# Performance work log

Hardware: AMD Instinct MI355X
Metric: run time of the kernel (lower is better)

The kernel has to match this reference:

```python
import jax, jax.numpy as jnp
import numpy as np

H = 1024   # hidden_size
F = 2048   # feature_length (encoder steps)
V = 50257  # output vocab size


def setup_inputs() -> dict:
    key = jax.random.key(0)
    ks = jax.random.split(key, 16)
    s = 0.02
    return {
        "input_tok": jax.random.randint(ks[0], (1,), 0, V, dtype=jnp.int32),
        "hidden": jax.random.normal(ks[1], (1, 1, H), dtype=jnp.float32),
        "encoder_output": jax.random.normal(ks[2], (1, F, H), dtype=jnp.float32),
        "emb": jax.random.normal(ks[3], (V, H), dtype=jnp.float32) * s,
        "attn_W": jax.random.normal(ks[4], (F, 2 * H), dtype=jnp.float32) * s,
        "attn_b": jnp.zeros((F,), dtype=jnp.float32),
        "comb_W": jax.random.normal(ks[5], (H, 2 * H), dtype=jnp.float32) * s,
        "comb_b": jnp.zeros((H,), dtype=jnp.float32),
        "W_ih": jax.random.normal(ks[6], (3 * H, H), dtype=jnp.float32) * s,
        "W_hh": jax.random.normal(ks[7], (3 * H, H), dtype=jnp.float32) * s,
        "b_ih": jnp.zeros((3 * H,), dtype=jnp.float32),
        "b_hh": jnp.zeros((3 * H,), dtype=jnp.float32),
        "out_W": jax.random.normal(ks[8], (V, H), dtype=jnp.float32) * s,
        "out_b": jnp.zeros((V,), dtype=jnp.float32),
    }


def reference(input_tok, hidden, encoder_output, emb, attn_W, attn_b,
              comb_W, comb_b, W_ih, W_hh, b_ih, b_hh, out_W, out_b):
    # embedding lookup -> [1, H] (dropout is identity in eval mode)
    embedded = emb[input_tok]                                   # [1, H]
    h = hidden[0]                                               # [1, H]
    # attention weights over encoder steps
    cat1 = jnp.concatenate([embedded, h], axis=1)               # [1, 2H]
    attn_weights = jax.nn.softmax(cat1 @ attn_W.T + attn_b, axis=1)  # [1, F]
    # weighted sum of encoder outputs
    attn_applied = attn_weights @ encoder_output[0]             # [1, H]
    # combine + relu
    cat2 = jnp.concatenate([embedded, attn_applied], axis=1)    # [1, 2H]
    x = jax.nn.relu(cat2 @ comb_W.T + comb_b)                   # [1, H]
    # single GRU step (torch gate order: r, z, n)
    gx = x @ W_ih.T + b_ih                                      # [1, 3H]
    gh = h @ W_hh.T + b_hh                                      # [1, 3H]
    r = jax.nn.sigmoid(gx[:, :H] + gh[:, :H])
    z = jax.nn.sigmoid(gx[:, H:2 * H] + gh[:, H:2 * H])
    n = jnp.tanh(gx[:, 2 * H:] + r * gh[:, 2 * H:])
    h_new = (1.0 - z) * n + z * h                               # [1, H]
    # output projection + log-softmax
    out = jax.nn.log_softmax(h_new @ out_W.T + out_b, axis=1)   # [1, V]
    return out, h_new[None], attn_weights
```

## Files before the change

### kernel.cpp

```cpp
#include <hip/hip_runtime.h>
#include <math.h>

#define H 1024
#define F 2048
#define V 50257

#define WS_ATTNL   0
#define WS_APPLIED 2048
#define WS_X       3072
#define WS_HNEW    4096
#define WS_LOGITS  5120
#define WS_STATS   55380

__device__ __forceinline__ float wave_sum(float v) {
    #pragma unroll
    for (int off = 32; off > 0; off >>= 1) v += __shfl_xor(v, off, 64);
    return v;
}

__device__ __forceinline__ float dot4(float4 a, float4 b) {
    return a.x * b.x + a.y * b.y + a.z * b.z + a.w * b.w;
}

__global__ void k_attn(const int* __restrict__ tok_p, const float* __restrict__ hidden,
                       const float* __restrict__ emb, const float* __restrict__ attn_W,
                       const float* __restrict__ attn_b, float* __restrict__ logits) {
    const int wv = threadIdx.x >> 6, lane = threadIdx.x & 63;
    const int f = blockIdx.x * 4 + wv;
    const int tok = tok_p[0];
    const float4* e4 = (const float4*)(emb + (size_t)tok * H);
    const float4* h4 = (const float4*)hidden;
    const float4* row = (const float4*)(attn_W + (size_t)f * (2 * H));
    float acc = 0.f;
    #pragma unroll
    for (int k = lane; k < H / 4; k += 64) acc += dot4(e4[k], row[k]);
    #pragma unroll
    for (int k = lane; k < H / 4; k += 64) acc += dot4(h4[k], row[H / 4 + k]);
    acc = wave_sum(acc);
    if (lane == 0) logits[f] = acc + attn_b[f];
}

__global__ void k_softmax(const float* __restrict__ logits, float* __restrict__ weights,
                          float* __restrict__ applied) {
    __shared__ float red[16];
    __shared__ float bc;
    const int t = threadIdx.x, lane = t & 63, wv = t >> 6;
    applied[t] = 0.f;
    float x0 = logits[t], x1 = logits[t + 1024];
    float m = fmaxf(x0, x1);
    #pragma unroll
    for (int off = 32; off > 0; off >>= 1) m = fmaxf(m, __shfl_xor(m, off, 64));
    if (lane == 0) red[wv] = m;
    __syncthreads();
    if (t == 0) { float M = red[0]; for (int w = 1; w < 16; ++w) M = fmaxf(M, red[w]); bc = M; }
    __syncthreads();
    const float M = bc;
    float e0 = expf(x0 - M), e1 = expf(x1 - M);
    float s = wave_sum(e0 + e1);
    if (lane == 0) red[wv] = s;
    __syncthreads();
    if (t == 0) { float S = red[0]; for (int w = 1; w < 16; ++w) S += red[w]; bc = 1.f / S; }
    __syncthreads();
    const float inv = bc;
    weights[t] = e0 * inv;
    weights[t + 1024] = e1 * inv;
}

__global__ void k_attnapply(const float* __restrict__ weights, const float* __restrict__ enc,
                            float* __restrict__ applied) {
    const int h = blockIdx.x * 256 + threadIdx.x;
    const int f0 = blockIdx.y * 32;
    float acc = 0.f;
    #pragma unroll 8
    for (int f = f0; f < f0 + 32; ++f) acc += weights[f] * enc[(size_t)f * H + h];
    atomicAdd(&applied[h], acc);
}

__global__ void k_comb(const int* __restrict__ tok_p, const float* __restrict__ emb,
                       const float* __restrict__ applied, const float* __restrict__ comb_W,
                       const float* __restrict__ comb_b, float* __restrict__ x) {
    const int wv = threadIdx.x >> 6, lane = threadIdx.x & 63;
    const int i = blockIdx.x * 4 + wv;
    const int tok = tok_p[0];
    const float4* e4 = (const float4*)(emb + (size_t)tok * H);
    const float4* a4 = (const float4*)applied;
    const float4* row = (const float4*)(comb_W + (size_t)i * (2 * H));
    float acc = 0.f;
    #pragma unroll
    for (int k = lane; k < H / 4; k += 64) acc += dot4(e4[k], row[k]);
    #pragma unroll
    for (int k = lane; k < H / 4; k += 64) acc += dot4(a4[k], row[H / 4 + k]);
    acc = wave_sum(acc);
    if (lane == 0) x[i] = fmaxf(acc + comb_b[i], 0.f);
}

__global__ void k_gru(const float* __restrict__ x, const float* __restrict__ hidden,
                      const float* __restrict__ W_ih, const float* __restrict__ W_hh,
                      const float* __restrict__ b_ih, const float* __restrict__ b_hh,
                      float* __restrict__ hnew_out, float* __restrict__ hnew_ws) {
    const int wv = threadIdx.x >> 6, lane = threadIdx.x & 63;
    const int i = blockIdx.x * 4 + wv;
    const float4* x4 = (const float4*)x;
    const float4* h4 = (const float4*)hidden;
    const float4* wri = (const float4*)(W_ih + (size_t)i * H);
    const float4* wzi = (const float4*)(W_ih + (size_t)(H + i) * H);
    const float4* wni = (const float4*)(W_ih + (size_t)(2 * H + i) * H);
    const float4* wrh = (const float4*)(W_hh + (size_t)i * H);
    const float4* wzh = (const float4*)(W_hh + (size_t)(H + i) * H);
    const float4* wnh = (const float4*)(W_hh + (size_t)(2 * H + i) * H);
    float ar = 0.f, az = 0.f, an = 0.f, br = 0.f, bz = 0.f, bn = 0.f;
    #pragma unroll
    for (int k = lane; k < H / 4; k += 64) {
        float4 xv = x4[k], hv = h4[k];
        ar += dot4(xv, wri[k]);
        az += dot4(xv, wzi[k]);
        an += dot4(xv, wni[k]);
        br += dot4(hv, wrh[k]);
        bz += dot4(hv, wzh[k]);
        bn += dot4(hv, wnh[k]);
    }
    ar = wave_sum(ar); az = wave_sum(az); an = wave_sum(an);
    br = wave_sum(br); bz = wave_sum(bz); bn = wave_sum(bn);
    if (lane == 0) {
        float r = 1.f / (1.f + expf(-((ar + b_ih[i]) + (br + b_hh[i]))));
        float z = 1.f / (1.f + expf(-((az + b_ih[H + i]) + (bz + b_hh[H + i]))));
        float n = tanhf((an + b_ih[2 * H + i]) + r * (bn + b_hh[2 * H + i]));
        float hn = (1.f - z) * n + z * hidden[i];
        hnew_out[i] = hn;
        hnew_ws[i] = hn;
    }
}

__global__ void k_out(const float* __restrict__ hnew, const float* __restrict__ out_W,
                      const float* __restrict__ out_b, float* __restrict__ logits) {
    const int wv = threadIdx.x >> 6, lane = threadIdx.x & 63;
    const int v = blockIdx.x * 4 + wv;
    if (v >= V) return;
    const float4* h4 = (const float4*)hnew;
    const float4* row = (const float4*)(out_W + (size_t)v * H);
    float acc = 0.f;
    #pragma unroll
    for (int k = lane; k < H / 4; k += 64) acc += dot4(h4[k], row[k]);
    acc = wave_sum(acc);
    if (lane == 0) logits[v] = acc + out_b[v];
}

__global__ void k_lsmreduce(const float* __restrict__ logits, float* __restrict__ stats) {
    __shared__ float sm[16], sl[16];
    const int t = threadIdx.x, lane = t & 63, wv = t >> 6;
    float m = -INFINITY, l = 0.f;
    for (int v = t; v < V; v += 1024) {
        float xv = logits[v];
        float mn = fmaxf(m, xv);
        l = l * expf(m - mn) + expf(xv - mn);
        m = mn;
    }
    #pragma unroll
    for (int off = 32; off > 0; off >>= 1) {
        float mo = __shfl_xor(m, off, 64);
        float lo = __shfl_xor(l, off, 64);
        float mn = fmaxf(m, mo);
        l = l * expf(m - mn) + lo * expf(mo - mn);
        m = mn;
    }
    if (lane == 0) { sm[wv] = m; sl[wv] = l; }
    __syncthreads();
    if (t == 0) {
        float M = sm[0], L = sl[0];
        for (int w = 1; w < 16; ++w) {
            float mn = fmaxf(M, sm[w]);
            L = L * expf(M - mn) + sl[w] * expf(sm[w] - mn);
            M = mn;
        }
        stats[0] = M;
        stats[1] = logf(L);
    }
}

__global__ void k_lsmwrite(const float* __restrict__ logits, const float* __restrict__ stats,
                           float* __restrict__ out) {
    const int v = blockIdx.x * 256 + threadIdx.x;
    if (v < V) out[v] = logits[v] - stats[0] - stats[1];
}

extern "C" void kernel_launch(void* const* d_in, const int* in_sizes, int n_in,
                              void* d_out, int out_size, void* d_ws, size_t ws_size,
                              hipStream_t stream) {
    const int*   tok    = (const int*)d_in[0];
    const float* hidden = (const float*)d_in[1];
    const float* enc    = (const float*)d_in[2];
    const float* emb    = (const float*)d_in[3];
    const float* attn_W = (const float*)d_in[4];
    const float* attn_b = (const float*)d_in[5];
    const float* comb_W = (const float*)d_in[6];
    const float* comb_b = (const float*)d_in[7];
    const float* W_ih   = (const float*)d_in[8];
    const float* W_hh   = (const float*)d_in[9];
    const float* b_ih   = (const float*)d_in[10];
    const float* b_hh   = (const float*)d_in[11];
    const float* out_W  = (const float*)d_in[12];
    const float* out_b  = (const float*)d_in[13];

    float* out        = (float*)d_out;
    float* out_hnew   = (float*)d_out + V;
    float* out_attnw  = (float*)d_out + V + H;
    float* ws         = (float*)d_ws;

    k_attn<<<F / 4, 256, 0, stream>>>(tok, hidden, emb, attn_W, attn_b, ws + WS_ATTNL);
    k_softmax<<<1, 1024, 0, stream>>>(ws + WS_ATTNL, out_attnw, ws + WS_APPLIED);
    k_attnapply<<<dim3(H / 256, F / 32), 256, 0, stream>>>(out_attnw, enc, ws + WS_APPLIED);
    k_comb<<<H / 4, 256, 0, stream>>>(tok, emb, ws + WS_APPLIED, comb_W, comb_b, ws + WS_X);
    k_gru<<<H / 4, 256, 0, stream>>>(ws + WS_X, hidden, W_ih, W_hh, b_ih, b_hh,
                                     out_hnew, ws + WS_HNEW);
    k_out<<<(V + 3) / 4, 256, 0, stream>>>(ws + WS_HNEW, out_W, out_b, ws + WS_LOGITS);
    k_lsmreduce<<<1, 1024, 0, stream>>>(ws + WS_LOGITS, ws + WS_STATS);
    k_lsmwrite<<<(V + 255) / 256, 256, 0, stream>>>(ws + WS_LOGITS, ws + WS_STATS, out);
}
```

Measured before the change: 451.2 us.

## Fuse softmax reductions into producers and overlap hidden-state GEMV with attention

Attention logits are exponentiated directly and partial sums are accumulated atomically, removing the single-block softmax kernel. Normalization is applied inside the attention-apply kernel. The W_hh projection runs in the same launch as the attention logits. The output projection processes four vocab rows per wave and accumulates exp sums, replacing the single-block log-softmax reduction. Dropping max subtraction risks overflow for large logits, and float atomics make sums nondeterministic.

```diff
diff --git a/kernel.cpp b/kernel.cpp
--- a/kernel.cpp
+++ b/kernel.cpp
@@ -5,12 +5,14 @@
 #define F 2048
 #define V 50257
 
-#define WS_ATTNL   0
-#define WS_APPLIED 2048
-#define WS_X       3072
-#define WS_HNEW    4096
-#define WS_LOGITS  5120
-#define WS_STATS   55380
+#define WS_ASUM    0
+#define WS_OSUM    64
+#define WS_EXPW    128
+#define WS_APPLIED 2176
+#define WS_X       3200
+#define WS_HNEW    4224
+#define WS_GH      5248
+#define WS_LOGITS  8320
 
 __device__ __forceinline__ float wave_sum(float v) {
     #pragma unroll
@@ -22,165 +24,146 @@
     return a.x * b.x + a.y * b.y + a.z * b.z + a.w * b.w;
 }
 
-__global__ void k_attn(const int* __restrict__ tok_p, const float* __restrict__ hidden,
-                       const float* __restrict__ emb, const float* __restrict__ attn_W,
-                       const float* __restrict__ attn_b, float* __restrict__ logits) {
-    const int wv = threadIdx.x >> 6, lane = threadIdx.x & 63;
-    const int f = blockIdx.x * 4 + wv;
-    const int tok = tok_p[0];
-    const float4* e4 = (const float4*)(emb + (size_t)tok * H);
+__global__ void k1_attn_gh(const int* __restrict__ tok_p, const float* __restrict__ hidden,
+                           const float* __restrict__ emb, const float* __restrict__ attn_W,
+                           const float* __restrict__ attn_b, const float* __restrict__ W_hh,
+                           const float* __restrict__ b_hh, float* __restrict__ ws) {
+    const int wv = threadIdx.x >> 6, lane = threadIdx.x & 63;
+    const int bid = blockIdx.x;
     const float4* h4 = (const float4*)hidden;
-    const float4* row = (const float4*)(attn_W + (size_t)f * (2 * H));
-    float acc = 0.f;
-    #pragma unroll
-    for (int k = lane; k < H / 4; k += 64) acc += dot4(e4[k], row[k]);
-    #pragma unroll
-    for (int k = lane; k < H / 4; k += 64) acc += dot4(h4[k], row[H / 4 + k]);
-    acc = wave_sum(acc);
-    if (lane == 0) logits[f] = acc + attn_b[f];
-}
-
-__global__ void k_softmax(const float* __restrict__ logits, float* __restrict__ weights,
-                          float* __restrict__ applied) {
-    __shared__ float red[16];
-    __shared__ float bc;
-    const int t = threadIdx.x, lane = t & 63, wv = t >> 6;
-    applied[t] = 0.f;
-    float x0 = logits[t], x1 = logits[t + 1024];
-    float m = fmaxf(x0, x1);
-    #pragma unroll
-    for (int off = 32; off > 0; off >>= 1) m = fmaxf(m, __shfl_xor(m, off, 64));
-    if (lane == 0) red[wv] = m;
-    __syncthreads();
-    if (t == 0) { float M = red[0]; for (int w = 1; w < 16; ++w) M = fmaxf(M, red[w]); bc = M; }
-    __syncthreads();
-    const float M = bc;
-    float e0 = expf(x0 - M), e1 = expf(x1 - M);
-    float s = wave_sum(e0 + e1);
-    if (lane == 0) red[wv] = s;
-    __syncthreads();
-    if (t == 0) { float S = red[0]; for (int w = 1; w < 16; ++w) S += red[w]; bc = 1.f / S; }
-    __syncthreads();
-    const float inv = bc;
-    weights[t] = e0 * inv;
-    weights[t + 1024] = e1 * inv;
-}
-
-__global__ void k_attnapply(const float* __restrict__ weights, const float* __restrict__ enc,
-                            float* __restrict__ applied) {
+    if (bid < F / 4) {
+        __shared__ float se[4];
+        const int f = bid * 4 + wv;
+        const int tok = tok_p[0];
+        const float4* e4 = (const float4*)(emb + (size_t)tok * H);
+        const float4* row = (const float4*)(attn_W + (size_t)f * (2 * H));
+        float acc = 0.f;
+        #pragma unroll
+        for (int k = lane; k < H / 4; k += 64)
+            acc += dot4(e4[k], row[k]) + dot4(h4[k], row[H / 4 + k]);
+        acc = wave_sum(acc);
+        if (lane == 0) {
+            float e = expf(acc + attn_b[f]);
+            ws[WS_EXPW + f] = e;
+            se[wv] = e;
+        }
+        __syncthreads();
+        if (threadIdx.x == 0)
+            atomicAdd(&ws[WS_ASUM + (bid & 63)], se[0] + se[1] + se[2] + se[3]);
+    } else {
+        const int i = (bid - F / 4) * 4 + wv;
+        const float4* row = (const float4*)(W_hh + (size_t)i * H);
+        float acc = 0.f;
+        #pragma unroll
+        for (int k = lane; k < H / 4; k += 64) acc += dot4(h4[k], row[k]);
+        acc = wave_sum(acc);
+        if (lane == 0) ws[WS_GH + i] = acc + b_hh[i];
+    }
+}
+
+__global__ void k2_apply(const float* __restrict__ enc, float* __restrict__ ws,
+                         float* __restrict__ out_attnw) {
     const int h = blockIdx.x * 256 + threadIdx.x;
     const int f0 = blockIdx.y * 32;
+    float s = 0.f;
+    #pragma unroll
+    for (int j = 0; j < 64; ++j) s += ws[WS_ASUM + j];
+    const float inv = 1.f / s;
     float acc = 0.f;
     #pragma unroll 8
-    for (int f = f0; f < f0 + 32; ++f) acc += weights[f] * enc[(size_t)f * H + h];
-    atomicAdd(&applied[h], acc);
-}
-
-__global__ void k_comb(const int* __restrict__ tok_p, const float* __restrict__ emb,
-                       const float* __restrict__ applied, const float* __restrict__ comb_W,
-                       const float* __restrict__ comb_b, float* __restrict__ x) {
+    for (int f = f0; f < f0 + 32; ++f) acc += ws[WS_EXPW + f] * enc[(size_t)f * H + h];
+    atomicAdd(&ws[WS_APPLIED + h], acc * inv);
+    if (blockIdx.x == 0 && threadIdx.x < 32) {
+        int f = f0 + threadIdx.x;
+        out_attnw[f] = ws[WS_EXPW + f] * inv;
+    }
+}
+
+__global__ void k3_comb(const int* __restrict__ tok_p, const float* __restrict__ emb,
+                        const float* __restrict__ comb_W, const float* __restrict__ comb_b,
+                        float* __restrict__ ws) {
     const int wv = threadIdx.x >> 6, lane = threadIdx.x & 63;
     const int i = blockIdx.x * 4 + wv;
     const int tok = tok_p[0];
     const float4* e4 = (const float4*)(emb + (size_t)tok * H);
-    const float4* a4 = (const float4*)applied;
+    const float4* a4 = (const float4*)(ws + WS_APPLIED);
     const float4* row = (const float4*)(comb_W + (size_t)i * (2 * H));
     float acc = 0.f;
     #pragma unroll
-    for (int k = lane; k < H / 4; k += 64) acc += dot4(e4[k], row[k]);
-    #pragma unroll
-    for (int k = lane; k < H / 4; k += 64) acc += dot4(a4[k], row[H / 4 + k]);
+    for (int k = lane; k < H / 4; k += 64)
+        acc += dot4(e4[k], row[k]) + dot4(a4[k], row[H / 4 + k]);
     acc = wave_sum(acc);
-    if (lane == 0) x[i] = fmaxf(acc + comb_b[i], 0.f);
-}
-
-__global__ void k_gru(const float* __restrict__ x, const float* __restrict__ hidden,
-                      const float* __restrict__ W_ih, const float* __restrict__ W_hh,
-                      const float* __restrict__ b_ih, const float* __restrict__ b_hh,
-                      float* __restrict__ hnew_out, float* __restrict__ hnew_ws) {
+    if (lane == 0) ws[WS_X + i] = fmaxf(acc + comb_b[i], 0.f);
+}
+
+__global__ void k4_gru(const float* __restrict__ hidden, const float* __restrict__ W_ih,
+                       const float* __restrict__ b_ih, float* __restrict__ ws,
+                       float* __restrict__ hnew_out) {
     const int wv = threadIdx.x >> 6, lane = threadIdx.x & 63;
     const int i = blockIdx.x * 4 + wv;
-    const float4* x4 = (const float4*)x;
-    const float4* h4 = (const float4*)hidden;
-    const float4* wri = (const float4*)(W_ih + (size_t)i * H);
-    const float4* wzi = (const float4*)(W_ih + (size_t)(H + i) * H);
-    const float4* wni = (const float4*)(W_ih + (size_t)(2 * H + i) * H);
-    const float4* wrh = (const float4*)(W_hh + (size_t)i * H);
-    const float4* wzh = (const float4*)(W_hh + (size_t)(H + i) * H);
-    const float4* wnh = (const float4*)(W_hh + (size_t)(2 * H + i) * H);
-    float ar = 0.f, az = 0.f, an = 0.f, br = 0.f, bz = 0.f, bn = 0.f;
+    const float4* x4 = (const float4*)(ws + WS_X);
+    const float4* wr = (const float4*)(W_ih + (size_t)i * H);
+    const float4* wz = (const float4*)(W_ih + (size_t)(H + i) * H);
+    const float4* wn = (const float4*)(W_ih + (size_t)(2 * H + i) * H);
+    float ar = 0.f, az = 0.f, an = 0.f;
     #pragma unroll
     for (int k = lane; k < H / 4; k += 64) {
-        float4 xv = x4[k], hv = h4[k];
-        ar += dot4(xv, wri[k]);
-        az += dot4(xv, wzi[k]);
-        an += dot4(xv, wni[k]);
-        br += dot4(hv, wrh[k]);
-        bz += dot4(hv, wzh[k]);
-        bn += dot4(hv, wnh[k]);
+        float4 xv = x4[k];
+        ar += dot4(xv, wr[k]);
+        az += dot4(xv, wz[k]);
+        an += dot4(xv, wn[k]);
     }
     ar = wave_sum(ar); az = wave_sum(az); an = wave_sum(an);
-    br = wave_sum(br); bz = wave_sum(bz); bn = wave_sum(bn);
     if (lane == 0) {
-        float r = 1.f / (1.f + expf(-((ar + b_ih[i]) + (br + b_hh[i]))));
-        float z = 1.f / (1.f + expf(-((az + b_ih[H + i]) + (bz + b_hh[H + i]))));
-        float n = tanhf((an + b_ih[2 * H + i]) + r * (bn + b_hh[2 * H + i]));
+        float r = 1.f / (1.f + expf(-((ar + b_ih[i]) + ws[WS_GH + i])));
+        float z = 1.f / (1.f + expf(-((az + b_ih[H + i]) + ws[WS_GH + H + i])));
+        float n = tanhf((an + b_ih[2 * H + i]) + r * ws[WS_GH + 2 * H + i]);
         float hn = (1.f - z) * n + z * hidden[i];
         hnew_out[i] = hn;
-        hnew_ws[i] = hn;
-    }
-}
-
-__global__ void k_out(const float* __restrict__ hnew, const float* __restrict__ out_W,
-                      const float* __restrict__ out_b, float* __restrict__ logits) {
-    const int wv = threadIdx.x >> 6, lane = threadIdx.x & 63;
-    const int v = blockIdx.x * 4 + wv;
-    if (v >= V) return;
-    const float4* h4 = (const float4*)hnew;
-    const float4* row = (const float4*)(out_W + (size_t)v * H);
-    float acc = 0.f;
-    #pragma unroll
-    for (int k = lane; k < H / 4; k += 64) acc += dot4(h4[k], row[k]);
-    acc = wave_sum(acc);
-    if (lane == 0) logits[v] = acc + out_b[v];
-}
-
-__global__ void k_lsmreduce(const float* __restrict__ logits, float* __restrict__ stats) {
-    __shared__ float sm[16], sl[16];
-    const int t = threadIdx.x, lane = t & 63, wv = t >> 6;
-    float m = -INFINITY, l = 0.f;
-    for (int v = t; v < V; v += 1024) {
-        float xv = logits[v];
-        float mn = fmaxf(m, xv);
-        l = l * expf(m - mn) + expf(xv - mn);
-        m = mn;
-    }
-    #pragma unroll
-    for (int off = 32; off > 0; off >>= 1) {
-        float mo = __shfl_xor(m, off, 64);
-        float lo = __shfl_xor(l, off, 64);
-        float mn = fmaxf(m, mo);
-        l = l * expf(m - mn) + lo * expf(mo - mn);
-        m = mn;
-    }
-    if (lane == 0) { sm[wv] = m; sl[wv] = l; }
+        ws[WS_HNEW + i] = hn;
+    }
+}
+
+__global__ void k5_out(const float* __restrict__ out_W, const float* __restrict__ out_b,
+                       float* __restrict__ ws) {
+    const int wv = threadIdx.x >> 6, lane = threadIdx.x & 63;
+    const int v0 = (blockIdx.x * 4 + wv) * 4;
+    __shared__ float se[4];
+    const float4* h4 = (const float4*)(ws + WS_HNEW);
+    const bool ok0 = v0 < V, ok1 = v0 + 1 < V, ok2 = v0 + 2 < V, ok3 = v0 + 3 < V;
+    const float4* r0 = (const float4*)(out_W + (size_t)(ok0 ? v0 : 0) * H);
+    const float4* r1 = (const float4*)(out_W + (size_t)(ok1 ? v0 + 1 : 0) * H);
+    const float4* r2 = (const float4*)(out_W + (size_t)(ok2 ? v0 + 2 : 0) * H);
+    const float4* r3 = (const float4*)(out_W + (size_t)(ok3 ? v0 + 3 : 0) * H);
+    float a0 = 0.f, a1 = 0.f, a2 = 0.f, a3 = 0.f;
+    #pragma unroll
+    for (int k = lane; k < H / 4; k += 64) {
+        float4 hv = h4[k];
+        a0 += dot4(hv, r0[k]);
+        a1 += dot4(hv, r1[k]);
+        a2 += dot4(hv, r2[k]);
+        a3 += dot4(hv, r3[k]);
+    }
+    a0 = wave_sum(a0); a1 = wave_sum(a1); a2 = wave_sum(a2); a3 = wave_sum(a3);
+    if (lane == 0) {
+        float es = 0.f, l;
+        if (ok0) { l = a0 + out_b[v0];     ws[WS_LOGITS + v0]     = l; es += expf(l); }
+        if (ok1) { l = a1 + out_b[v0 + 1]; ws[WS_LOGITS + v0 + 1] = l; es += expf(l); }
+        if (ok2) { l = a2 + out_b[v0 + 2]; ws[WS_LOGITS + v0 + 2] = l; es += expf(l); }
+        if (ok3) { l = a3 + out_b[v0 + 3]; ws[WS_LOGITS + v0 + 3] = l; es += expf(l); }
+        se[wv] = es;
+    }
     __syncthreads();
-    if (t == 0) {
-        float M = sm[0], L = sl[0];
-        for (int w = 1; w < 16; ++w) {
-            float mn = fmaxf(M, sm[w]);
-            L = L * expf(M - mn) + sl[w] * expf(sm[w] - mn);
-            M = mn;
-        }
-        stats[0] = M;
-        stats[1] = logf(L);
-    }
-}
-
-__global__ void k_lsmwrite(const float* __restrict__ logits, const float* __restrict__ stats,
-                           float* __restrict__ out) {
+    if (threadIdx.x == 0)
+        atomicAdd(&ws[WS_OSUM + (blockIdx.x & 63)], se[0] + se[1] + se[2] + se[3]);
+}
+
+__global__ void k6_lsm(const float* __restrict__ ws, float* __restrict__ out) {
     const int v = blockIdx.x * 256 + threadIdx.x;
-    if (v < V) out[v] = logits[v] - stats[0] - stats[1];
+    float s = 0.f;
+    #pragma unroll
+    for (int j = 0; j < 64; ++j) s += ws[WS_OSUM + j];
+    if (v < V) out[v] = ws[WS_LOGITS + v] - logf(s);
 }
 
 extern "C" void kernel_launch(void* const* d_in, const int* in_sizes, int n_in,
@@ -201,18 +184,18 @@
     const float* out_W  = (const float*)d_in[12];
     const float* out_b  = (const float*)d_in[13];
 
-    float* out        = (float*)d_out;
-    float* out_hnew   = (float*)d_out + V;
-    float* out_attnw  = (float*)d_out + V + H;
-    float* ws         = (float*)d_ws;
-
-    k_attn<<<F / 4, 256, 0, stream>>>(tok, hidden, emb, attn_W, attn_b, ws + WS_ATTNL);
-    k_softmax<<<1, 1024, 0, stream>>>(ws + WS_ATTNL, out_attnw, ws + WS_APPLIED);
-    k_attnapply<<<dim3(H / 256, F / 32), 256, 0, stream>>>(out_attnw, enc, ws + WS_APPLIED);
-    k_comb<<<H / 4, 256, 0, stream>>>(tok, emb, ws + WS_APPLIED, comb_W, comb_b, ws + WS_X);
-    k_gru<<<H / 4, 256, 0, stream>>>(ws + WS_X, hidden, W_ih, W_hh, b_ih, b_hh,
-                                     out_hnew, ws + WS_HNEW);
-    k_out<<<(V + 3) / 4, 256, 0, stream>>>(ws + WS_HNEW, out_W, out_b, ws + WS_LOGITS);
-    k_lsmreduce<<<1, 1024, 0, stream>>>(ws + WS_LOGITS, ws + WS_STATS);
-    k_lsmwrite<<<(V + 255) / 256, 256, 0, stream>>>(ws + WS_LOGITS, ws + WS_STATS, out);
-}
+    float* out       = (float*)d_out;
+    float* out_hnew  = (float*)d_out + V;
+    float* out_attnw = (float*)d_out + V + H;
+    float* ws        = (float*)d_ws;
+
+    hipMemsetAsync(d_ws, 0, (size_t)WS_X * sizeof(float), stream);
+
+    k1_attn_gh<<<F / 4 + (3 * H) / 4, 256, 0, stream>>>(tok, hidden, emb, attn_W, attn_b,
+                                                        W_hh, b_hh, ws);
+    k2_apply<<<dim3(H / 256, F / 32), 256, 0, stream>>>(enc, ws, out_attnw);
+    k3_comb<<<H / 4, 256, 0, stream>>>(tok, emb, comb_W, comb_b, ws);
+    k4_gru<<<H / 4, 256, 0, stream>>>(hidden, W_ih, b_ih, ws, out_hnew);
+    k5_out<<<(V + 15) / 16, 256, 0, stream>>>(out_W, out_b, ws);
+    k6_lsm<<<(V + 255) / 256, 256, 0, stream>>>(ws, out);
+}
```

Result: faster. 431.3 us (-4.4%).
